# Kernel optimization log

Measured on AMD Instinct MI355X. Metric: run time of the kernel, lower is better.

Reference implementation:

```python
import jax, jax.numpy as jnp
import numpy as np

BETA = 0.9          # snn.Leaky default-ish decay given in module
THRESH = 1.0        # snntorch default threshold


def spike(x):
    # heaviside(x); surrogate grad handled in bwd module
    return (x > 0).astype(x.dtype)


def setup_inputs() -> dict:
    key = jax.random.key(0)
    ks = jax.random.split(key, 5)
    T, B, NI, NH, NO = 100, 512, 784, 1024, 10
    x = jax.random.normal(ks[0], (T, B, NI), dtype=jnp.float32)
    W1 = jax.random.normal(ks[1], (NH, NI), dtype=jnp.float32) / np.sqrt(NI)
    b1 = jax.random.normal(ks[2], (NH,), dtype=jnp.float32) * 0.01
    W2 = jax.random.normal(ks[3], (NO, NH), dtype=jnp.float32) / np.sqrt(NH)
    b2 = jax.random.normal(ks[4], (NO,), dtype=jnp.float32) * 0.01
    return {"x": x, "W1": W1, "b1": b1, "W2": W2, "b2": b2}


def reference(x, W1, b1, W2, b2):
    # x: [T, B, num_inputs]
    B = x.shape[1]
    NH = W1.shape[0]
    NO = W2.shape[0]
    dt = x.dtype

    def step(carry, xt):
        mem1, mem2 = carry
        cur1 = xt @ W1.T + b1                       # [B, NH]
        reset1 = (mem1 > THRESH).astype(dt)         # from previous mem
        mem1 = BETA * mem1 + cur1 - reset1 * THRESH
        spk1 = spike(mem1 - THRESH)
        cur2 = spk1 @ W2.T + b2                     # [B, NO]
        reset2 = (mem2 > THRESH).astype(dt)
        mem2 = BETA * mem2 + cur2 - reset2 * THRESH
        spk2 = spike(mem2 - THRESH)
        return (mem1, mem2), spk2

    init = (jnp.zeros((B, NH), dt), jnp.zeros((B, NO), dt))
    (_, mem2), spk2_rec = jax.lax.scan(step, init, x)
    return spk2_rec, mem2
```

## Files before the change

kernel.cpp:

```cpp
#include <hip/hip_runtime.h>
#include <hip/hip_bf16.h>

#define NI 784
#define NH 1024
#define NO 10
#define BATCH 512
#define TSTEPS 100

#define BM 128
#define BN 128
#define BK 16
#define LDT 132
#define TCH 10

typedef __attribute__((ext_vector_type(4))) float floatx4;

__global__ __launch_bounds__(256) void init_ws_kernel(float* __restrict__ p, int n) {
  int i = blockIdx.x * 256 + threadIdx.x;
  if (i < n) p[i] = 0.0f;
}

__global__ __launch_bounds__(256) void sgemm1_kernel(
    const float* __restrict__ X,
    const float* __restrict__ W1,
    const float* __restrict__ b1,
    float* __restrict__ C)
{
  __shared__ __align__(16) float As[BK * LDT];
  __shared__ __align__(16) float Bs[BK * LDT];

  const int tid = threadIdx.x;
  const int tx = tid & 15;
  const int ty = tid >> 4;

  const int hb    = blockIdx.y * gridDim.x + blockIdx.x;
  const int chunk = (gridDim.x * gridDim.y) >> 3;
  const int f     = (hb & 7) * chunk + (hb >> 3);
  const int n0 = (f & 7) * BN;
  const int m0 = (f >> 3) * BM;

  const int srow  = tid >> 2;
  const int skcol = (tid & 3) * 4;

  float acc[8][8];
#pragma unroll
  for (int i = 0; i < 8; ++i)
#pragma unroll
    for (int j = 0; j < 8; ++j) acc[i][j] = 0.0f;

  const float* Xs  = X  + (size_t)m0 * NI + skcol;
  const float* W1s = W1 + (size_t)n0 * NI + skcol;

  floatx4 xa0 = *(const floatx4*)&Xs [(size_t)(srow)      * NI];
  floatx4 xa1 = *(const floatx4*)&Xs [(size_t)(64 + srow) * NI];
  floatx4 wq0 = *(const floatx4*)&W1s[(size_t)(srow)      * NI];
  floatx4 wq1 = *(const floatx4*)&W1s[(size_t)(64 + srow) * NI];

  for (int kt = 0; kt < NI / BK; ++kt) {
    __syncthreads();
#pragma unroll
    for (int e = 0; e < 4; ++e) {
      As[(skcol + e) * LDT + srow]      = xa0[e];
      As[(skcol + e) * LDT + 64 + srow] = xa1[e];
      Bs[(skcol + e) * LDT + srow]      = wq0[e];
      Bs[(skcol + e) * LDT + 64 + srow] = wq1[e];
    }
    __syncthreads();

    if (kt + 1 < NI / BK) {
      const int k0 = (kt + 1) * BK;
      xa0 = *(const floatx4*)&Xs [(size_t)(srow)      * NI + k0];
      xa1 = *(const floatx4*)&Xs [(size_t)(64 + srow) * NI + k0];
      wq0 = *(const floatx4*)&W1s[(size_t)(srow)      * NI + k0];
      wq1 = *(const floatx4*)&W1s[(size_t)(64 + srow) * NI + k0];
    }

#pragma unroll
    for (int k = 0; k < BK; ++k) {
      const floatx4 av0 = *(const floatx4*)&As[k * LDT + ty * 8];
      const floatx4 av1 = *(const floatx4*)&As[k * LDT + ty * 8 + 4];
      const floatx4 bv0 = *(const floatx4*)&Bs[k * LDT + tx * 4];
      const floatx4 bv1 = *(const floatx4*)&Bs[k * LDT + 64 + tx * 4];
      const float a[8] = {av0[0], av0[1], av0[2], av0[3],
                          av1[0], av1[1], av1[2], av1[3]};
#pragma unroll
      for (int i = 0; i < 8; ++i)
#pragma unroll
        for (int j = 0; j < 4; ++j) {
          acc[i][j]     = fmaf(a[i], bv0[j], acc[i][j]);
          acc[i][4 + j] = fmaf(a[i], bv1[j], acc[i][4 + j]);
        }
    }
  }

#pragma unroll
  for (int i = 0; i < 8; ++i) {
    const int m = m0 + ty * 8 + i;
    floatx4 v0, v1;
#pragma unroll
    for (int j = 0; j < 4; ++j) {
      v0[j] = acc[i][j]     + b1[n0 + tx * 4 + j];
      v1[j] = acc[i][4 + j] + b1[n0 + 64 + tx * 4 + j];
    }
    *(floatx4*)&C[(size_t)m * NH + n0 + tx * 4]      = v0;
    *(floatx4*)&C[(size_t)m * NH + n0 + 64 + tx * 4] = v1;
  }
}

__global__ __launch_bounds__(64) void spk1_kernel(
    const float* __restrict__ cur1,
    unsigned long long* __restrict__ spk)
{
  const int b  = blockIdx.x;
  const int qq = blockIdx.y;
  const int l  = threadIdx.x;

  const floatx4* c4 = (const floatx4*)cur1;
  const size_t stride = (size_t)BATCH * (NH / 4);
  const size_t base   = (size_t)b * (NH / 4) + qq * 64 + l;

  floatx4 m1 = {0.f, 0.f, 0.f, 0.f};
  floatx4 c  = c4[base];
  floatx4 c1 = c4[base + stride];

  for (int t = 0; t < TSTEPS; ++t) {
    floatx4 c2 = {0.f, 0.f, 0.f, 0.f};
    if (t + 2 < TSTEPS) c2 = c4[base + (size_t)(t + 2) * stride];

    unsigned long long bm0 = 0, bm1 = 0, bm2 = 0, bm3 = 0;
#pragma unroll
    for (int j = 0; j < 4; ++j) {
      float mj = m1[j];
      float reset = (mj > 1.0f) ? 1.0f : 0.0f;
      mj = 0.9f * mj + c[j] - reset;
      m1[j] = mj;
      unsigned long long bm = __ballot(mj > 1.0f);
      if (j == 0) bm0 = bm; else if (j == 1) bm1 = bm;
      else if (j == 2) bm2 = bm; else bm3 = bm;
    }

    if (l < 4) {
      unsigned long long v = bm0;
      if (l == 1) v = bm1;
      else if (l == 2) v = bm2;
      else if (l == 3) v = bm3;
      spk[((size_t)t * BATCH + b) * 16 + qq * 4 + l] = v;
    }
    c = c1; c1 = c2;
  }
}

__global__ __launch_bounds__(256) void cur2_kernel(
    const unsigned long long* __restrict__ spk,
    const float* __restrict__ W2,
    const float* __restrict__ b2,
    float* __restrict__ cur2T)
{
  const int b   = blockIdx.x;
  const int t0  = blockIdx.y * TCH;
  const int tid = threadIdx.x;
  const int lane = tid & 63;
  const int wave = tid >> 6;

  __shared__ float red[2][4][NO];

  float w[4][NO];
#pragma unroll
  for (int j = 0; j < 4; ++j)
#pragma unroll
    for (int o = 0; o < NO; ++o)
      w[j][o] = W2[o * NH + tid * 4 + j];

  float bb = 0.0f;
  if (tid < NO) bb = b2[tid];

  for (int t = t0; t < t0 + TCH; ++t) {
    const unsigned long long* pk = spk + ((size_t)t * BATCH + b) * 16 + wave * 4;
    const unsigned long long p0 = pk[0], p1 = pk[1], p2 = pk[2], p3 = pk[3];

    float a[NO];
#pragma unroll
    for (int o = 0; o < NO; ++o) a[o] = 0.0f;

    {
      const float s0 = (float)((p0 >> lane) & 1ULL);
#pragma unroll
      for (int o = 0; o < NO; ++o) a[o] = fmaf(s0, w[0][o], a[o]);
      const float s1 = (float)((p1 >> lane) & 1ULL);
#pragma unroll
      for (int o = 0; o < NO; ++o) a[o] = fmaf(s1, w[1][o], a[o]);
      const float s2 = (float)((p2 >> lane) & 1ULL);
#pragma unroll
      for (int o = 0; o < NO; ++o) a[o] = fmaf(s2, w[2][o], a[o]);
      const float s3 = (float)((p3 >> lane) & 1ULL);
#pragma unroll
      for (int o = 0; o < NO; ++o) a[o] = fmaf(s3, w[3][o], a[o]);
    }

#pragma unroll
    for (int m = 1; m <= 32; m <<= 1)
#pragma unroll
      for (int o = 0; o < NO; ++o) a[o] += __shfl_xor(a[o], m, 64);

    if (lane == 0) {
#pragma unroll
      for (int o = 0; o < NO; ++o) red[t & 1][wave][o] = a[o];
    }
    __syncthreads();

    if (tid < NO) {
      float cur2 = red[t & 1][0][tid] + red[t & 1][1][tid]
                 + red[t & 1][2][tid] + red[t & 1][3][tid] + bb;
      cur2T[((size_t)b * NO + tid) * TSTEPS + t] = cur2;
    }
  }
}

__global__ __launch_bounds__(256) void mem2_kernel(
    const float* __restrict__ cur2T,
    float* __restrict__ out,
    long long out_size)
{
  const int id = blockIdx.x * 256 + threadIdx.x;
  if (id >= BATCH * NO) return;
  const int b = id / NO;
  const int o = id % NO;
  const float* row = cur2T + (size_t)id * TSTEPS;

  float m2 = 0.0f;
#pragma unroll
  for (int t = 0; t < TSTEPS; t += 4) {
    const floatx4 v = *(const floatx4*)&row[t];
#pragma unroll
    for (int e = 0; e < 4; ++e) {
      float reset2 = (m2 > 1.0f) ? 1.0f : 0.0f;
      m2 = 0.9f * m2 + v[e] - reset2;
      float spk2 = (m2 > 1.0f) ? 1.0f : 0.0f;
      long long idx = ((long long)(t + e) * BATCH + b) * NO + o;
      if (idx < out_size) out[idx] = spk2;
    }
  }
  long long idx = (long long)TSTEPS * BATCH * NO + id;
  if (idx < out_size) out[idx] = m2;
}

__global__ __launch_bounds__(256) void recur_kernel(
    const float* __restrict__ cur1,
    const float* __restrict__ W2,
    const float* __restrict__ b2,
    float* __restrict__ mem1s,
    float* __restrict__ mem2s,
    float* __restrict__ out,
    long long out_size, int t0, int tc, int last)
{
  const int b    = blockIdx.x;
  const int tid  = threadIdx.x;
  const int lane = tid & 63;
  const int wave = tid >> 6;

  __shared__ float red[4][NO];

  float w[4][NO];
#pragma unroll
  for (int j = 0; j < 4; ++j)
#pragma unroll
    for (int o = 0; o < NO; ++o)
      w[j][o] = W2[o * NH + tid * 4 + j];

  floatx4 m1 = *(const floatx4*)&mem1s[(size_t)b * NH + tid * 4];
  float m2 = 0.0f, bb = 0.0f;
  if (tid < NO) {
    m2 = mem2s[b * NO + tid];
    bb = b2[tid];
  }

  const floatx4* c4 = (const floatx4*)cur1;
  floatx4 c = c4[((size_t)0 * BATCH + b) * (NH / 4) + tid];

  for (int t = 0; t < tc; ++t) {
    floatx4 cn = {0.f, 0.f, 0.f, 0.f};
    if (t + 1 < tc) cn = c4[((size_t)(t + 1) * BATCH + b) * (NH / 4) + tid];

    float a[NO];
#pragma unroll
    for (int o = 0; o < NO; ++o) a[o] = 0.0f;

#pragma unroll
    for (int j = 0; j < 4; ++j) {
      float mj = m1[j];
      float reset = (mj > 1.0f) ? 1.0f : 0.0f;
      mj = 0.9f * mj + c[j] - reset;
      m1[j] = mj;
      float s = (mj > 1.0f) ? 1.0f : 0.0f;
#pragma unroll
      for (int o = 0; o < NO; ++o) a[o] = fmaf(s, w[j][o], a[o]);
    }

#pragma unroll
    for (int m = 1; m <= 32; m <<= 1)
#pragma unroll
      for (int o = 0; o < NO; ++o) a[o] += __shfl_xor(a[o], m, 64);

    if (lane == 0) {
#pragma unroll
      for (int o = 0; o < NO; ++o) red[wave][o] = a[o];
    }
    __syncthreads();

    if (tid < NO) {
      float cur2 = red[0][tid] + red[1][tid] + red[2][tid] + red[3][tid] + bb;
      float reset2 = (m2 > 1.0f) ? 1.0f : 0.0f;
      m2 = 0.9f * m2 + cur2 - reset2;
      float spk2 = (m2 > 1.0f) ? 1.0f : 0.0f;
      long long idx = ((long long)(t0 + t) * BATCH + b) * NO + tid;
      if (idx < out_size) out[idx] = spk2;
    }
    __syncthreads();
    c = cn;
  }

  *(floatx4*)&mem1s[(size_t)b * NH + tid * 4] = m1;
  if (tid < NO) {
    mem2s[b * NO + tid] = m2;
    if (last) {
      long long idx = (long long)TSTEPS * BATCH * NO + b * NO + tid;
      if (idx < out_size) out[idx] = m2;
    }
  }
}

__global__ __launch_bounds__(256) void fused_fp32_kernel(
    const float* __restrict__ x,
    const float* __restrict__ W1,
    const float* __restrict__ b1,
    const float* __restrict__ W2,
    const float* __restrict__ b2,
    float* __restrict__ out, long long out_size)
{
  const int b    = blockIdx.x;
  const int tid  = threadIdx.x;
  const int lane = tid & 63;
  const int wave = tid >> 6;

  __shared__ __align__(16) float xs[NI + 4];
  __shared__ float red[4][NO];

  float w[4][NO];
#pragma unroll
  for (int j = 0; j < 4; ++j)
#pragma unroll
    for (int o = 0; o < NO; ++o)
      w[j][o] = W2[o * NH + tid * 4 + j];

  float bias1[4];
#pragma unroll
  for (int j = 0; j < 4; ++j) bias1[j] = b1[tid * 4 + j];

  float m1[4] = {0.f, 0.f, 0.f, 0.f};
  float m2 = 0.0f, bb = 0.0f;
  if (tid < NO) bb = b2[tid];

  for (int t = 0; t < TSTEPS; ++t) {
    if (tid < 196)
      *(floatx4*)&xs[tid * 4] = *(const floatx4*)&x[((size_t)t * BATCH + b) * NI + tid * 4];
    __syncthreads();

    float a[NO];
#pragma unroll
    for (int o = 0; o < NO; ++o) a[o] = 0.0f;

#pragma unroll
    for (int j = 0; j < 4; ++j) {
      const float* wr = W1 + (size_t)(tid * 4 + j) * NI;
      float dot = 0.0f;
      for (int cch = 0; cch < 196; ++cch) {
        floatx4 wv = *(const floatx4*)&wr[cch * 4];
        floatx4 xv = *(const floatx4*)&xs[cch * 4];
#pragma unroll
        for (int e = 0; e < 4; ++e) dot = fmaf(wv[e], xv[e], dot);
      }
      float cur = dot + bias1[j];
      float mj = m1[j];
      float reset = (mj > 1.0f) ? 1.0f : 0.0f;
      mj = 0.9f * mj + cur - reset;
      m1[j] = mj;
      float s = (mj > 1.0f) ? 1.0f : 0.0f;
#pragma unroll
      for (int o = 0; o < NO; ++o) a[o] = fmaf(s, w[j][o], a[o]);
    }

#pragma unroll
    for (int m = 1; m <= 32; m <<= 1)
#pragma unroll
      for (int o = 0; o < NO; ++o) a[o] += __shfl_xor(a[o], m, 64);

    if (lane == 0) {
#pragma unroll
      for (int o = 0; o < NO; ++o) red[wave][o] = a[o];
    }
    __syncthreads();

    if (tid < NO) {
      float cur2 = red[0][tid] + red[1][tid] + red[2][tid] + red[3][tid] + bb;
      float reset2 = (m2 > 1.0f) ? 1.0f : 0.0f;
      m2 = 0.9f * m2 + cur2 - reset2;
      float spk2 = (m2 > 1.0f) ? 1.0f : 0.0f;
      long long idx = ((long long)t * BATCH + b) * NO + tid;
      if (idx < out_size) out[idx] = spk2;
    }
    __syncthreads();
  }

  if (tid < NO) {
    long long idx = (long long)TSTEPS * BATCH * NO + b * NO + tid;
    if (idx < out_size) out[idx] = m2;
  }
}

extern "C" void kernel_launch(void* const* d_in, const int* in_sizes, int n_in,
                              void* d_out, int out_size, void* d_ws, size_t ws_size,
                              hipStream_t stream) {
  const float* x  = (const float*)d_in[0];
  const float* W1 = (const float*)d_in[1];
  const float* b1 = (const float*)d_in[2];
  const float* W2 = (const float*)d_in[3];
  const float* b2 = (const float*)d_in[4];
  float* out = (float*)d_out;

  char* ws = (char*)d_ws;

  const size_t cur2T_bytes = (size_t)BATCH * NO * TSTEPS * 4;
  const size_t head        = (cur2T_bytes + 255) & ~(size_t)255;
  const size_t cur1_bytes  = (size_t)TSTEPS * BATCH * NH * 4;
  const size_t pack_bytes  = (size_t)TSTEPS * BATCH * 16 * 8;
  const size_t need_full   = head + cur1_bytes + pack_bytes;

  if (d_ws != nullptr && ws_size >= need_full) {
    float* cur2T = (float*)ws;
    float* cur1  = (float*)(ws + head);
    unsigned long long* spk = (unsigned long long*)(ws + head + cur1_bytes);

    dim3 g(NH / BN, (TSTEPS * BATCH) / BM);
    sgemm1_kernel<<<g, 256, 0, stream>>>(x, W1, b1, cur1);
    spk1_kernel<<<dim3(BATCH, 4), 64, 0, stream>>>(cur1, spk);
    cur2_kernel<<<dim3(BATCH, TSTEPS / TCH), 256, 0, stream>>>(spk, W2, b2, cur2T);
    mem2_kernel<<<(BATCH * NO + 255) / 256, 256, 0, stream>>>(cur2T, out,
                                                              (long long)out_size);
    return;
  }

  const size_t mem1_bytes = (size_t)BATCH * NH * 4;
  const size_t mem2_bytes = (size_t)BATCH * NO * 4;
  size_t fixed = (mem1_bytes + mem2_bytes + 255) & ~(size_t)255;
  const size_t per_step = (size_t)BATCH * NH * 4;

  if (d_ws == nullptr || ws_size < fixed + per_step) {
    fused_fp32_kernel<<<BATCH, 256, 0, stream>>>(x, W1, b1, W2, b2, out,
                                                 (long long)out_size);
    return;
  }

  float* mem1s = (float*)ws;
  float* mem2s = (float*)(ws + mem1_bytes);
  float* cur1  = (float*)(ws + fixed);

  int Tc = (int)((ws_size - fixed) / per_step);
  if (Tc > TSTEPS) Tc = TSTEPS;

  const int nInit = BATCH * NH + BATCH * NO;
  init_ws_kernel<<<(nInit + 255) / 256, 256, 0, stream>>>((float*)ws, nInit);

  for (int t0 = 0; t0 < TSTEPS; t0 += Tc) {
    const int tc = (TSTEPS - t0 < Tc) ? (TSTEPS - t0) : Tc;
    const int M = tc * BATCH;
    dim3 g(NH / BN, M / BM);
    sgemm1_kernel<<<g, 256, 0, stream>>>(x + (size_t)t0 * BATCH * NI, W1, b1, cur1);
    recur_kernel<<<BATCH, 256, 0, stream>>>(cur1, W2, b2, mem1s, mem2s, out,
                                            (long long)out_size, t0, tc,
                                            (t0 + tc >= TSTEPS) ? 1 : 0);
  }
}
```

Measured before the change: 1.317 ms.

## Fuse spike, cur2 and mem2 phases into one per-batch kernel

Replaces the three post-GEMM kernels (spk1, cur2, mem2) with one phases_kernel per batch row. Spike bitmasks and cur2 values now stay in shared memory, so the global round trips and two launches go away. It also changes the GEMM LDS padding (LDT 132 to 140). The trade-off is less parallelism: the spike phase now has 512 blocks of 256 threads instead of 2048 blocks of 64, the cur2 phase runs 100 serial steps per block instead of being split across 10 time chunks, and the prefetch depth drops to one step.

```diff
diff --git a/kernel.cpp b/kernel.cpp
--- a/kernel.cpp
+++ b/kernel.cpp
@@ -10,8 +10,7 @@
 #define BM 128
 #define BN 128
 #define BK 16
-#define LDT 132
-#define TCH 10
+#define LDT 140
 
 typedef __attribute__((ext_vector_type(4))) float floatx4;
 
@@ -107,141 +106,125 @@
   }
 }
 
-__global__ __launch_bounds__(64) void spk1_kernel(
+__global__ __launch_bounds__(256) void phases_kernel(
     const float* __restrict__ cur1,
-    unsigned long long* __restrict__ spk)
-{
-  const int b  = blockIdx.x;
-  const int qq = blockIdx.y;
-  const int l  = threadIdx.x;
-
-  const floatx4* c4 = (const floatx4*)cur1;
-  const size_t stride = (size_t)BATCH * (NH / 4);
-  const size_t base   = (size_t)b * (NH / 4) + qq * 64 + l;
-
-  floatx4 m1 = {0.f, 0.f, 0.f, 0.f};
-  floatx4 c  = c4[base];
-  floatx4 c1 = c4[base + stride];
-
-  for (int t = 0; t < TSTEPS; ++t) {
-    floatx4 c2 = {0.f, 0.f, 0.f, 0.f};
-    if (t + 2 < TSTEPS) c2 = c4[base + (size_t)(t + 2) * stride];
-
-    unsigned long long bm0 = 0, bm1 = 0, bm2 = 0, bm3 = 0;
-#pragma unroll
-    for (int j = 0; j < 4; ++j) {
-      float mj = m1[j];
-      float reset = (mj > 1.0f) ? 1.0f : 0.0f;
-      mj = 0.9f * mj + c[j] - reset;
-      m1[j] = mj;
-      unsigned long long bm = __ballot(mj > 1.0f);
-      if (j == 0) bm0 = bm; else if (j == 1) bm1 = bm;
-      else if (j == 2) bm2 = bm; else bm3 = bm;
-    }
-
-    if (l < 4) {
-      unsigned long long v = bm0;
-      if (l == 1) v = bm1;
-      else if (l == 2) v = bm2;
-      else if (l == 3) v = bm3;
-      spk[((size_t)t * BATCH + b) * 16 + qq * 4 + l] = v;
-    }
-    c = c1; c1 = c2;
-  }
-}
-
-__global__ __launch_bounds__(256) void cur2_kernel(
-    const unsigned long long* __restrict__ spk,
     const float* __restrict__ W2,
     const float* __restrict__ b2,
-    float* __restrict__ cur2T)
-{
-  const int b   = blockIdx.x;
-  const int t0  = blockIdx.y * TCH;
-  const int tid = threadIdx.x;
-  const int lane = tid & 63;
-  const int wave = tid >> 6;
-
-  __shared__ float red[2][4][NO];
-
-  float w[4][NO];
-#pragma unroll
-  for (int j = 0; j < 4; ++j)
-#pragma unroll
-    for (int o = 0; o < NO; ++o)
-      w[j][o] = W2[o * NH + tid * 4 + j];
-
-  float bb = 0.0f;
-  if (tid < NO) bb = b2[tid];
-
-  for (int t = t0; t < t0 + TCH; ++t) {
-    const unsigned long long* pk = spk + ((size_t)t * BATCH + b) * 16 + wave * 4;
-    const unsigned long long p0 = pk[0], p1 = pk[1], p2 = pk[2], p3 = pk[3];
-
-    float a[NO];
-#pragma unroll
-    for (int o = 0; o < NO; ++o) a[o] = 0.0f;
-
-    {
-      const float s0 = (float)((p0 >> lane) & 1ULL);
-#pragma unroll
-      for (int o = 0; o < NO; ++o) a[o] = fmaf(s0, w[0][o], a[o]);
-      const float s1 = (float)((p1 >> lane) & 1ULL);
-#pragma unroll
-      for (int o = 0; o < NO; ++o) a[o] = fmaf(s1, w[1][o], a[o]);
-      const float s2 = (float)((p2 >> lane) & 1ULL);
-#pragma unroll
-      for (int o = 0; o < NO; ++o) a[o] = fmaf(s2, w[2][o], a[o]);
-      const float s3 = (float)((p3 >> lane) & 1ULL);
-#pragma unroll
-      for (int o = 0; o < NO; ++o) a[o] = fmaf(s3, w[3][o], a[o]);
-    }
-
-#pragma unroll
-    for (int m = 1; m <= 32; m <<= 1)
-#pragma unroll
-      for (int o = 0; o < NO; ++o) a[o] += __shfl_xor(a[o], m, 64);
-
-    if (lane == 0) {
-#pragma unroll
-      for (int o = 0; o < NO; ++o) red[t & 1][wave][o] = a[o];
-    }
-    __syncthreads();
-
-    if (tid < NO) {
-      float cur2 = red[t & 1][0][tid] + red[t & 1][1][tid]
-                 + red[t & 1][2][tid] + red[t & 1][3][tid] + bb;
-      cur2T[((size_t)b * NO + tid) * TSTEPS + t] = cur2;
-    }
-  }
-}
-
-__global__ __launch_bounds__(256) void mem2_kernel(
-    const float* __restrict__ cur2T,
     float* __restrict__ out,
     long long out_size)
 {
-  const int id = blockIdx.x * 256 + threadIdx.x;
-  if (id >= BATCH * NO) return;
-  const int b = id / NO;
-  const int o = id % NO;
-  const float* row = cur2T + (size_t)id * TSTEPS;
-
-  float m2 = 0.0f;
-#pragma unroll
-  for (int t = 0; t < TSTEPS; t += 4) {
-    const floatx4 v = *(const floatx4*)&row[t];
-#pragma unroll
-    for (int e = 0; e < 4; ++e) {
+  const int b    = blockIdx.x;
+  const int tid  = threadIdx.x;
+  const int lane = tid & 63;
+  const int wave = tid >> 6;
+
+  __shared__ unsigned long long sp[TSTEPS][16];
+  __shared__ float c2s[TSTEPS][NO];
+  __shared__ float red[2][4][NO];
+
+  {
+    const floatx4* c4 = (const floatx4*)cur1;
+    const size_t stride = (size_t)BATCH * (NH / 4);
+    const size_t base   = (size_t)b * (NH / 4) + wave * 64 + lane;
+
+    floatx4 m1 = {0.f, 0.f, 0.f, 0.f};
+    floatx4 c  = c4[base];
+
+    for (int t = 0; t < TSTEPS; ++t) {
+      floatx4 cn = {0.f, 0.f, 0.f, 0.f};
+      if (t + 1 < TSTEPS) cn = c4[base + (size_t)(t + 1) * stride];
+
+      unsigned long long bm0 = 0, bm1 = 0, bm2 = 0, bm3 = 0;
+#pragma unroll
+      for (int j = 0; j < 4; ++j) {
+        float mj = m1[j];
+        float reset = (mj > 1.0f) ? 1.0f : 0.0f;
+        mj = 0.9f * mj + c[j] - reset;
+        m1[j] = mj;
+        unsigned long long bm = __ballot(mj > 1.0f);
+        if (j == 0) bm0 = bm; else if (j == 1) bm1 = bm;
+        else if (j == 2) bm2 = bm; else bm3 = bm;
+      }
+
+      if (lane < 4) {
+        unsigned long long v = bm0;
+        if (lane == 1) v = bm1;
+        else if (lane == 2) v = bm2;
+        else if (lane == 3) v = bm3;
+        sp[t][wave * 4 + lane] = v;
+      }
+      c = cn;
+    }
+  }
+  __syncthreads();
+
+  {
+    float w[4][NO];
+#pragma unroll
+    for (int j = 0; j < 4; ++j)
+#pragma unroll
+      for (int o = 0; o < NO; ++o)
+        w[j][o] = W2[o * NH + tid * 4 + j];
+
+    float bb = 0.0f;
+    if (tid < NO) bb = b2[tid];
+
+    for (int t = 0; t < TSTEPS; ++t) {
+      const unsigned long long p0 = sp[t][wave * 4 + 0];
+      const unsigned long long p1 = sp[t][wave * 4 + 1];
+      const unsigned long long p2 = sp[t][wave * 4 + 2];
+      const unsigned long long p3 = sp[t][wave * 4 + 3];
+
+      float a[NO];
+#pragma unroll
+      for (int o = 0; o < NO; ++o) a[o] = 0.0f;
+
+      {
+        const float s0 = (float)((p0 >> lane) & 1ULL);
+#pragma unroll
+        for (int o = 0; o < NO; ++o) a[o] = fmaf(s0, w[0][o], a[o]);
+        const float s1 = (float)((p1 >> lane) & 1ULL);
+#pragma unroll
+        for (int o = 0; o < NO; ++o) a[o] = fmaf(s1, w[1][o], a[o]);
+        const float s2 = (float)((p2 >> lane) & 1ULL);
+#pragma unroll
+        for (int o = 0; o < NO; ++o) a[o] = fmaf(s2, w[2][o], a[o]);
+        const float s3 = (float)((p3 >> lane) & 1ULL);
+#pragma unroll
+        for (int o = 0; o < NO; ++o) a[o] = fmaf(s3, w[3][o], a[o]);
+      }
+
+#pragma unroll
+      for (int m = 1; m <= 32; m <<= 1)
+#pragma unroll
+        for (int o = 0; o < NO; ++o) a[o] += __shfl_xor(a[o], m, 64);
+
+      if (lane == 0) {
+#pragma unroll
+        for (int o = 0; o < NO; ++o) red[t & 1][wave][o] = a[o];
+      }
+      __syncthreads();
+
+      if (tid < NO) {
+        c2s[t][tid] = red[t & 1][0][tid] + red[t & 1][1][tid]
+                    + red[t & 1][2][tid] + red[t & 1][3][tid] + bb;
+      }
+    }
+  }
+  __syncthreads();
+
+  if (tid < NO) {
+    float m2 = 0.0f;
+    for (int t = 0; t < TSTEPS; ++t) {
       float reset2 = (m2 > 1.0f) ? 1.0f : 0.0f;
-      m2 = 0.9f * m2 + v[e] - reset2;
+      m2 = 0.9f * m2 + c2s[t][tid] - reset2;
       float spk2 = (m2 > 1.0f) ? 1.0f : 0.0f;
-      long long idx = ((long long)(t + e) * BATCH + b) * NO + o;
+      long long idx = ((long long)t * BATCH + b) * NO + tid;
       if (idx < out_size) out[idx] = spk2;
     }
-  }
-  long long idx = (long long)TSTEPS * BATCH * NO + id;
-  if (idx < out_size) out[idx] = m2;
+    long long idx = (long long)TSTEPS * BATCH * NO + b * NO + tid;
+    if (idx < out_size) out[idx] = m2;
+  }
 }
 
 __global__ __launch_bounds__(256) void recur_kernel(
@@ -429,23 +412,15 @@
 
   char* ws = (char*)d_ws;
 
-  const size_t cur2T_bytes = (size_t)BATCH * NO * TSTEPS * 4;
-  const size_t head        = (cur2T_bytes + 255) & ~(size_t)255;
-  const size_t cur1_bytes  = (size_t)TSTEPS * BATCH * NH * 4;
-  const size_t pack_bytes  = (size_t)TSTEPS * BATCH * 16 * 8;
-  const size_t need_full   = head + cur1_bytes + pack_bytes;
-
-  if (d_ws != nullptr && ws_size >= need_full) {
-    float* cur2T = (float*)ws;
-    float* cur1  = (float*)(ws + head);
-    unsigned long long* spk = (unsigned long long*)(ws + head + cur1_bytes);
+  const size_t cur1_bytes = (size_t)TSTEPS * BATCH * NH * 4;
+
+  if (d_ws != nullptr && ws_size >= cur1_bytes) {
+    float* cur1 = (float*)ws;
 
     dim3 g(NH / BN, (TSTEPS * BATCH) / BM);
     sgemm1_kernel<<<g, 256, 0, stream>>>(x, W1, b1, cur1);
-    spk1_kernel<<<dim3(BATCH, 4), 64, 0, stream>>>(cur1, spk);
-    cur2_kernel<<<dim3(BATCH, TSTEPS / TCH), 256, 0, stream>>>(spk, W2, b2, cur2T);
-    mem2_kernel<<<(BATCH * NO + 255) / 256, 256, 0, stream>>>(cur2T, out,
-                                                              (long long)out_size);
+    phases_kernel<<<BATCH, 256, 0, stream>>>(cur1, W2, b2, out,
+                                             (long long)out_size);
     return;
   }
 
```

Result: faster. 1.280 ms (-2.8%).

## Double-buffer shared tiles in SGEMM1 and shorten spk1 prefetch depth

Applied to the files above, without the earlier changes.

The first GEMM now ping-pongs between two shared-memory tile buffers, which removes one of the two barriers per K-step and lets global prefetch and LDS staging overlap with compute on the other buffer. The LDS row pitch changes from 132 to 140 floats, and the inner FMA loop is regrouped by A half. Separately, the membrane-update kernel prefetches one timestep ahead instead of two, which lowers register pressure but hides less load latency. The extra shared-memory buffers double LDS use per block and may reduce occupancy.

```diff
diff --git a/kernel.cpp b/kernel.cpp
--- a/kernel.cpp
+++ b/kernel.cpp
@@ -10,7 +10,7 @@
 #define BM 128
 #define BN 128
 #define BK 16
-#define LDT 132
+#define LDT 140
 #define TCH 10
 
 typedef __attribute__((ext_vector_type(4))) float floatx4;
@@ -26,8 +26,10 @@
     const float* __restrict__ b1,
     float* __restrict__ C)
 {
-  __shared__ __align__(16) float As[BK * LDT];
-  __shared__ __align__(16) float Bs[BK * LDT];
+  __shared__ __align__(16) float As0[BK * LDT];
+  __shared__ __align__(16) float Bs0[BK * LDT];
+  __shared__ __align__(16) float As1[BK * LDT];
+  __shared__ __align__(16) float Bs1[BK * LDT];
 
   const int tid = threadIdx.x;
   const int tx = tid & 15;
@@ -51,47 +53,69 @@
   const float* Xs  = X  + (size_t)m0 * NI + skcol;
   const float* W1s = W1 + (size_t)n0 * NI + skcol;
 
-  floatx4 xa0 = *(const floatx4*)&Xs [(size_t)(srow)      * NI];
-  floatx4 xa1 = *(const floatx4*)&Xs [(size_t)(64 + srow) * NI];
-  floatx4 wq0 = *(const floatx4*)&W1s[(size_t)(srow)      * NI];
-  floatx4 wq1 = *(const floatx4*)&W1s[(size_t)(64 + srow) * NI];
-
-  for (int kt = 0; kt < NI / BK; ++kt) {
-    __syncthreads();
-#pragma unroll
-    for (int e = 0; e < 4; ++e) {
-      As[(skcol + e) * LDT + srow]      = xa0[e];
-      As[(skcol + e) * LDT + 64 + srow] = xa1[e];
-      Bs[(skcol + e) * LDT + srow]      = wq0[e];
-      Bs[(skcol + e) * LDT + 64 + srow] = wq1[e];
-    }
-    __syncthreads();
-
-    if (kt + 1 < NI / BK) {
-      const int k0 = (kt + 1) * BK;
-      xa0 = *(const floatx4*)&Xs [(size_t)(srow)      * NI + k0];
-      xa1 = *(const floatx4*)&Xs [(size_t)(64 + srow) * NI + k0];
-      wq0 = *(const floatx4*)&W1s[(size_t)(srow)      * NI + k0];
-      wq1 = *(const floatx4*)&W1s[(size_t)(64 + srow) * NI + k0];
-    }
-
-#pragma unroll
-    for (int k = 0; k < BK; ++k) {
-      const floatx4 av0 = *(const floatx4*)&As[k * LDT + ty * 8];
-      const floatx4 av1 = *(const floatx4*)&As[k * LDT + ty * 8 + 4];
-      const floatx4 bv0 = *(const floatx4*)&Bs[k * LDT + tx * 4];
-      const floatx4 bv1 = *(const floatx4*)&Bs[k * LDT + 64 + tx * 4];
-      const float a[8] = {av0[0], av0[1], av0[2], av0[3],
-                          av1[0], av1[1], av1[2], av1[3]};
-#pragma unroll
-      for (int i = 0; i < 8; ++i)
-#pragma unroll
-        for (int j = 0; j < 4; ++j) {
-          acc[i][j]     = fmaf(a[i], bv0[j], acc[i][j]);
-          acc[i][4 + j] = fmaf(a[i], bv1[j], acc[i][4 + j]);
-        }
-    }
-  }
+  floatx4 xa0, xa1, wq0, wq1;
+
+#define PREFETCH(KT)                                                  \
+  {                                                                   \
+    const int k0_ = (KT) * BK;                                        \
+    xa0 = *(const floatx4*)&Xs [(size_t)(srow)      * NI + k0_];      \
+    xa1 = *(const floatx4*)&Xs [(size_t)(64 + srow) * NI + k0_];      \
+    wq0 = *(const floatx4*)&W1s[(size_t)(srow)      * NI + k0_];      \
+    wq1 = *(const floatx4*)&W1s[(size_t)(64 + srow) * NI + k0_];      \
+  }
+
+#define STAGE(Abuf, Bbuf)                                             \
+  _Pragma("unroll")                                                   \
+  for (int e = 0; e < 4; ++e) {                                       \
+    Abuf[(skcol + e) * LDT + srow]      = xa0[e];                     \
+    Abuf[(skcol + e) * LDT + 64 + srow] = xa1[e];                     \
+    Bbuf[(skcol + e) * LDT + srow]      = wq0[e];                     \
+    Bbuf[(skcol + e) * LDT + 64 + srow] = wq1[e];                     \
+  }
+
+#define COMPUTE(Abuf, Bbuf)                                           \
+  _Pragma("unroll")                                                   \
+  for (int k = 0; k < BK; ++k) {                                      \
+    const floatx4 av0 = *(const floatx4*)&Abuf[k * LDT + ty * 8];     \
+    const floatx4 av1 = *(const floatx4*)&Abuf[k * LDT + ty * 8 + 4]; \
+    const floatx4 bv0 = *(const floatx4*)&Bbuf[k * LDT + tx * 4];     \
+    const floatx4 bv1 = *(const floatx4*)&Bbuf[k * LDT + 64 + tx * 4];\
+    _Pragma("unroll")                                                 \
+    for (int i = 0; i < 4; ++i)                                       \
+      _Pragma("unroll")                                               \
+      for (int j = 0; j < 4; ++j) {                                   \
+        acc[i][j]     = fmaf(av0[i], bv0[j], acc[i][j]);              \
+        acc[i][4 + j] = fmaf(av0[i], bv1[j], acc[i][4 + j]);          \
+      }                                                               \
+    _Pragma("unroll")                                                 \
+    for (int i = 0; i < 4; ++i)                                       \
+      _Pragma("unroll")                                               \
+      for (int j = 0; j < 4; ++j) {                                   \
+        acc[4 + i][j]     = fmaf(av1[i], bv0[j], acc[4 + i][j]);      \
+        acc[4 + i][4 + j] = fmaf(av1[i], bv1[j], acc[4 + i][4 + j]);  \
+      }                                                               \
+  }
+
+  PREFETCH(0);
+  STAGE(As0, Bs0);
+  __syncthreads();
+
+  for (int kt = 0; kt < 48; kt += 2) {
+    PREFETCH(kt + 1);
+    COMPUTE(As0, Bs0);
+    STAGE(As1, Bs1);
+    __syncthreads();
+
+    PREFETCH(kt + 2);
+    COMPUTE(As1, Bs1);
+    STAGE(As0, Bs0);
+    __syncthreads();
+  }
+  COMPUTE(As0, Bs0);
+
+#undef PREFETCH
+#undef STAGE
+#undef COMPUTE
 
 #pragma unroll
   for (int i = 0; i < 8; ++i) {
@@ -121,11 +145,10 @@
 
   floatx4 m1 = {0.f, 0.f, 0.f, 0.f};
   floatx4 c  = c4[base];
-  floatx4 c1 = c4[base + stride];
 
   for (int t = 0; t < TSTEPS; ++t) {
-    floatx4 c2 = {0.f, 0.f, 0.f, 0.f};
-    if (t + 2 < TSTEPS) c2 = c4[base + (size_t)(t + 2) * stride];
+    floatx4 cn = {0.f, 0.f, 0.f, 0.f};
+    if (t + 1 < TSTEPS) cn = c4[base + (size_t)(t + 1) * stride];
 
     unsigned long long bm0 = 0, bm1 = 0, bm2 = 0, bm3 = 0;
 #pragma unroll
@@ -146,7 +169,7 @@
       else if (l == 3) v = bm3;
       spk[((size_t)t * BATCH + b) * 16 + qq * 4 + l] = v;
     }
-    c = c1; c1 = c2;
+    c = cn;
   }
 }
 
```

Measured after the change: 1.492 ms. 13.3% more time.
